# Performance work log

Hardware: AMD Instinct MI355X
Metric: run time of the kernel (lower is better)

Reference implementation:

```python
import jax, jax.numpy as jnp
import numpy as np

L_LAYERS = 6
D = 768
H = 12
DH = D // H
FF = 3072
B = 32
LX = 256
LY = 128
EPS = 1e-6
NEG = -1e9


def setup_inputs() -> dict:
    key = jax.random.key(0)
    ks = jax.random.split(key, 24)
    s = 0.02
    f32 = jnp.float32
    inp = {
        'y': jax.random.normal(ks[0], (B, LY, D), f32),
        'x': jax.random.normal(ks[1], (B, LX, D), f32),
        'y_mask': jnp.zeros((B, 1, 1, LY), bool),
        'x_mask': jnp.zeros((B, 1, 1, LX), bool),
        'y_pos': jnp.arange(B * LY, dtype=jnp.int32).reshape(B, LY),
        'bbox': jax.random.normal(ks[2], (B, LX, 4), f32),
        # encoder (SA) params, stacked over layers; attn weight order: q,k,v,merge
        'enc_attn_w': jax.random.normal(ks[3], (L_LAYERS, 4, D, D), f32) * s,
        'enc_attn_b': jnp.zeros((L_LAYERS, 4, D), f32),
        'enc_ffn_w1': jax.random.normal(ks[4], (L_LAYERS, D, FF), f32) * s,
        'enc_ffn_b1': jnp.zeros((L_LAYERS, FF), f32),
        'enc_ffn_w2': jax.random.normal(ks[5], (L_LAYERS, FF, D), f32) * s,
        'enc_ffn_b2': jnp.zeros((L_LAYERS, D), f32),
        'enc_ln_g': jnp.ones((L_LAYERS, 2, D), f32),
        'enc_ln_b': jnp.zeros((L_LAYERS, 2, D), f32),
        # decoder (RELAGA) params; two attentions per layer (self, cross)
        'dec_attn_w': jax.random.normal(ks[6], (L_LAYERS, 2, 4, D, D), f32) * s,
        'dec_attn_b': jnp.zeros((L_LAYERS, 2, 4, D), f32),
        'dec_ffn_w1': jax.random.normal(ks[7], (L_LAYERS, D, FF), f32) * s,
        'dec_ffn_b1': jnp.zeros((L_LAYERS, FF), f32),
        'dec_ffn_w2': jax.random.normal(ks[8], (L_LAYERS, FF, D), f32) * s,
        'dec_ffn_b2': jnp.zeros((L_LAYERS, D), f32),
        'dec_ln_g': jnp.ones((L_LAYERS, 3, D), f32),
        'dec_ln_b': jnp.zeros((L_LAYERS, 3, D), f32),
    }
    return inp


def _layernorm(t, g, b):
    m = jnp.mean(t, axis=-1, keepdims=True)
    v = jnp.mean((t - m) ** 2, axis=-1, keepdims=True)
    return g * (t - m) / jnp.sqrt(v + EPS) + b


def _heads(t, w, bias):
    # [B,L,D] -> [B,H,L,DH]
    nb = t.shape[0]
    return (t @ w + bias).reshape(nb, -1, H, DH).transpose(0, 2, 1, 3)


def _mha(v, k, q, mask, w, bias, rel=None):
    # w: [4,D,D] (q,k,v,merge), bias: [4,D]; rel: [B,1,Lq,Lq] or None
    qh = _heads(q, w[0], bias[0])
    kh = _heads(k, w[1], bias[1])
    vh = _heads(v, w[2], bias[2])
    scores = jnp.einsum('bhqd,bhkd->bhqk', qh, kh) / np.sqrt(DH).astype(np.float32)
    scores = jnp.where(mask, NEG, scores)
    att = jax.nn.softmax(scores, axis=-1)
    out = jnp.einsum('bhqk,bhkd->bhqd', att, vh)
    if rel is not None:
        out = jnp.einsum('bhqp,bhpd->bhqd', rel, out)  # bbox-relational matmul
    nb = q.shape[0]
    out = out.transpose(0, 2, 1, 3).reshape(nb, -1, D)
    return out @ w[3] + bias[3]


def _ffn(t, w1, b1, w2, b2):
    return jnp.maximum(t @ w1 + b1, 0.0) @ w2 + b2


def reference(y, x, y_mask, x_mask, y_pos, bbox,
              enc_attn_w, enc_attn_b, enc_ffn_w1, enc_ffn_b1, enc_ffn_w2, enc_ffn_b2,
              enc_ln_g, enc_ln_b,
              dec_attn_w, dec_attn_b, dec_ffn_w1, dec_ffn_b1, dec_ffn_w2, dec_ffn_b2,
              dec_ln_g, dec_ln_b):
    # bbox cosine-similarity relation matrix (softmax over last dim), shared across heads
    prod = jnp.einsum('bic,bjc->bij', bbox, bbox)
    n = jnp.sqrt(jnp.sum(bbox * bbox, axis=-1))          # [B,LX]
    denom = n[:, :, None] * n[:, None, :]                 # [B,LX,LX]
    sim = jax.nn.softmax(prod / denom, axis=2)[:, None]   # [B,1,LX,LX] broadcasts over heads

    for i in range(L_LAYERS):  # encoder: SA stack over y
        att = _mha(y, y, y, y_mask, enc_attn_w[i], enc_attn_b[i])
        y = _layernorm(y + att, enc_ln_g[i, 0], enc_ln_b[i, 0])
        f = _ffn(y, enc_ffn_w1[i], enc_ffn_b1[i], enc_ffn_w2[i], enc_ffn_b2[i])
        y = _layernorm(y + f, enc_ln_g[i, 1], enc_ln_b[i, 1])

    for i in range(L_LAYERS):  # decoder: RELAGA stack over x
        att = _mha(x, x, x, x_mask, dec_attn_w[i, 0], dec_attn_b[i, 0], rel=sim)
        x = _layernorm(x + att, dec_ln_g[i, 0], dec_ln_b[i, 0])
        att = _mha(y, y, x, y_mask, dec_attn_w[i, 1], dec_attn_b[i, 1], rel=sim)
        x = _layernorm(x + att, dec_ln_g[i, 1], dec_ln_b[i, 1])
        f = _ffn(x, dec_ffn_w1[i], dec_ffn_b1[i], dec_ffn_w2[i], dec_ffn_b2[i])
        x = _layernorm(x + f, dec_ln_g[i, 2], dec_ln_b[i, 2])

    return (y, x)
```

## Files before the change

### kernel.cpp

```cpp
#include <hip/hip_runtime.h>

#define DEV __device__ __forceinline__

constexpr int NB  = 32;
constexpr int LXc = 256;
constexpr int LYc = 128;
constexpr int Dc  = 768;
constexpr int NH  = 12;
constexpr int FFc = 3072;

typedef unsigned short u16;
typedef float f32x4 __attribute__((ext_vector_type(4)));
typedef short s16x8 __attribute__((ext_vector_type(8)));

DEV u16 f2bf(float f) {
  unsigned u = __float_as_uint(f);
  u += 0x7FFFu + ((u >> 16) & 1u);
  return (u16)(u >> 16);
}
DEV float bf2f(u16 w) { return __uint_as_float(((unsigned)w) << 16); }
DEV float ldf(const void* p, long long i, int isbf) {
  return isbf ? bf2f(((const u16*)p)[i]) : ((const float*)p)[i];
}

DEV void gload16(const void* g, void* l) {
  __builtin_amdgcn_global_load_lds(
      (const __attribute__((address_space(1))) void*)g,
      (__attribute__((address_space(3))) void*)l, 16, 0, 0);
}
DEV void barx() {
  asm volatile("" ::: "memory");
  __builtin_amdgcn_s_barrier();
  asm volatile("" ::: "memory");
}

__global__ void k_detect(const u16* y, int* flag) {
  if (threadIdx.x == 0) {
    int cnt = 0;
    for (int i = 0; i < 256; ++i) {
      u16 w = y[i];
      int e = (w >> 7) & 0xFF;
      if (e == 0 || (e >= 112 && e <= 140)) cnt++;
    }
    *flag = (cnt >= 200) ? 1 : 0;
  }
}

__global__ void k_ingest_b(const void* src, u16* dst, long long n, const int* flag) {
  int isbf = *flag;
  long long i = (long long)blockIdx.x * blockDim.x + threadIdx.x;
  long long st = (long long)gridDim.x * blockDim.x;
  for (; i < n; i += st) dst[i] = isbf ? ((const u16*)src)[i] : f2bf(((const float*)src)[i]);
}

__global__ void k_cvt(const void* src, float* dst, long long n, const int* flag) {
  int isbf = *flag;
  long long i = (long long)blockIdx.x * blockDim.x + threadIdx.x;
  long long st = (long long)gridDim.x * blockDim.x;
  for (; i < n; i += st) dst[i] = ldf(src, i, isbf);
}

__global__ void k_emit(const u16* ybuf, const u16* xbuf, void* out,
                       const int* flag, long long ny, long long nt) {
  int isbf = *flag;
  long long i = (long long)blockIdx.x * blockDim.x + threadIdx.x;
  long long st = (long long)gridDim.x * blockDim.x;
  for (; i < nt; i += st) {
    u16 v = (i < ny) ? ybuf[i] : xbuf[i - ny];
    if (isbf) ((u16*)out)[i] = v;
    else      ((float*)out)[i] = bf2f(v);
  }
}

__global__ __launch_bounds__(256) void k_wt(const void* src, u16* dst, int R, int C, const int* flag) {
  int isbf = *flag;
  __shared__ u16 t[32][33];
  long long base = (long long)blockIdx.z * R * C;
  int c0 = blockIdx.x * 32, r0 = blockIdx.y * 32;
  int tx = threadIdx.x & 31, ty = threadIdx.x >> 5;
#pragma unroll
  for (int k = 0; k < 4; ++k) {
    int r = r0 + ty + k * 8;
    t[ty + k * 8][tx] = f2bf(ldf(src, base + (long long)r * C + (c0 + tx), isbf));
  }
  __syncthreads();
#pragma unroll
  for (int k = 0; k < 4; ++k) {
    int c = c0 + ty + k * 8;
    dst[base + (long long)c * R + (r0 + tx)] = t[tx][ty + k * 8];
  }
}

__global__ __launch_bounds__(256) void k_bboxsim(const void* bbox, const int* flag, u16* sim) {
  int isbf = *flag;
  int b = blockIdx.x >> 8, i = blockIdx.x & 255;
  int j = threadIdx.x;
  long long base = (long long)b * LXc * 4;
  float a[4], c[4];
#pragma unroll
  for (int t = 0; t < 4; ++t) {
    a[t] = ldf(bbox, base + (long long)i * 4 + t, isbf);
    c[t] = ldf(bbox, base + (long long)j * 4 + t, isbf);
  }
  float dot = a[0]*c[0] + a[1]*c[1] + a[2]*c[2] + a[3]*c[3];
  float na  = sqrtf(a[0]*a[0] + a[1]*a[1] + a[2]*a[2] + a[3]*a[3]);
  float ncn = sqrtf(c[0]*c[0] + c[1]*c[1] + c[2]*c[2] + c[3]*c[3]);
  float v = dot / (na * ncn);
  __shared__ float r1[4], r2[4];
  float m = v;
  for (int o = 32; o; o >>= 1) m = fmaxf(m, __shfl_xor(m, o));
  if ((threadIdx.x & 63) == 0) r1[threadIdx.x >> 6] = m;
  __syncthreads();
  m = fmaxf(fmaxf(r1[0], r1[1]), fmaxf(r1[2], r1[3]));
  float e = __expf(v - m);
  float s = e;
  for (int o = 32; o; o >>= 1) s += __shfl_xor(s, o);
  if ((threadIdx.x & 63) == 0) r2[threadIdx.x >> 6] = s;
  __syncthreads();
  s = r2[0] + r2[1] + r2[2] + r2[3];
  sim[((long long)b * LXc + i) * LXc + j] = f2bf(e / s);
}

__global__ __launch_bounds__(192) void k_lnres4(u16* curb, const u16* delta,
                                                const void* g, long long gOff,
                                                const void* bb, long long bOff,
                                                const int* flag) {
  int isbf = *flag;
  long long row = blockIdx.x;
  u16* xr = curb + row * Dc;
  const u16* dr = delta + row * Dc;
  int t = threadIdx.x;
  union { u16 u[4]; uint2 d; } xa, da;
  xa.d = *(const uint2*)(xr + t * 4);
  da.d = *(const uint2*)(dr + t * 4);
  float v[4];
  float s = 0.f;
#pragma unroll
  for (int i = 0; i < 4; ++i) { v[i] = bf2f(xa.u[i]) + bf2f(da.u[i]); s += v[i]; }
  __shared__ float r1[3], r2[3];
  for (int o = 32; o; o >>= 1) s += __shfl_xor(s, o);
  if ((t & 63) == 0) r1[t >> 6] = s;
  __syncthreads();
  float mean = (r1[0] + r1[1] + r1[2]) * (1.0f / 768.0f);
  float s2 = 0.f;
#pragma unroll
  for (int i = 0; i < 4; ++i) { float d = v[i] - mean; s2 += d * d; }
  for (int o = 32; o; o >>= 1) s2 += __shfl_xor(s2, o);
  if ((t & 63) == 0) r2[t >> 6] = s2;
  __syncthreads();
  float var = (r2[0] + r2[1] + r2[2]) * (1.0f / 768.0f);
  float rstd = rsqrtf(var + 1e-6f);
  union { u16 u[4]; uint2 d; } oa;
#pragma unroll
  for (int i = 0; i < 4; ++i) {
    int c = t * 4 + i;
    float o = ldf(g, gOff + c, isbf) * (v[i] - mean) * rstd + ldf(bb, bOff + c, isbf);
    oa.u[i] = f2bf(o);
  }
  *(uint2*)(xr + t * 4) = oa.d;
}

template<int DEC>
__global__ __launch_bounds__(256) void k_attn(const u16* __restrict__ Q,
                                              const u16* __restrict__ Kb,
                                              const u16* __restrict__ Vt,
                                              u16* __restrict__ Out,
                                              int Lq, int Lk) {
  __shared__ __align__(16) u16 Kl[64 * 64];
  __shared__ __align__(16) u16 Vl[64 * 64];
  __shared__ __align__(16) u16 Pl[4][16][72];
  const int tid = threadIdx.x, wid = tid >> 6, lane = tid & 63;
  const int qt = blockIdx.x, h = blockIdx.y, b = blockIdx.z;
  const int q0 = qt * 64 + wid * 16;
  const int rl = lane & 15, sx = lane >> 4;
  const int srow = lane >> 3;
  const int scol8 = ((lane & 7) ^ srow) << 3;

  s16x8 qa[2];
  {
    const u16* qrow = Q + ((long long)b * Lq + q0 + rl) * Dc + h * 64;
    qa[0] = *(const s16x8*)(qrow + sx * 8);
    qa[1] = *(const s16x8*)(qrow + 32 + sx * 8);
  }
  f32x4 o[4] = {};
  float m[4], l[4];
#pragma unroll
  for (int e = 0; e < 4; ++e) { m[e] = -3.0e38f; l[e] = 0.f; }

  const long long kbase = (long long)b * Lk * Dc + h * 64;
  const long long vbase = ((long long)b * Dc + h * 64) * Lk;

  for (int k0 = 0; k0 < Lk; k0 += 64) {
#pragma unroll
    for (int g = 0; g < 2; ++g) {
      int chunk = g * 4 + wid;
      gload16(Kb + kbase + (long long)(k0 + chunk * 8 + srow) * Dc + scol8,
              (char*)Kl + chunk * 1024);
    }
#pragma unroll
    for (int g = 0; g < 2; ++g) {
      int chunk = g * 4 + wid;
      gload16(Vt + vbase + (long long)(chunk * 8 + srow) * Lk + k0 + scol8,
              (char*)Vl + chunk * 1024);
    }
    asm volatile("s_waitcnt vmcnt(0)" ::: "memory");
    barx();

    f32x4 s[4];
#pragma unroll
    for (int n = 0; n < 4; ++n) {
      s16x8 b0 = *(const s16x8*)((char*)Kl + (n * 16 + rl) * 128 + ((sx    ) ^ (rl & 7)) * 16);
      s16x8 b1 = *(const s16x8*)((char*)Kl + (n * 16 + rl) * 128 + ((sx + 4) ^ (rl & 7)) * 16);
      f32x4 acc = {};
      acc = __builtin_amdgcn_mfma_f32_16x16x32_bf16(qa[0], b0, acc, 0, 0, 0);
      acc = __builtin_amdgcn_mfma_f32_16x16x32_bf16(qa[1], b1, acc, 0, 0, 0);
      s[n] = acc;
    }
#pragma unroll
    for (int n = 0; n < 4; ++n)
#pragma unroll
      for (int e = 0; e < 4; ++e) s[n][e] *= 0.125f;

#pragma unroll
    for (int e = 0; e < 4; ++e) {
      float v = fmaxf(fmaxf(s[0][e], s[1][e]), fmaxf(s[2][e], s[3][e]));
      v = fmaxf(v, __shfl_xor(v, 1));
      v = fmaxf(v, __shfl_xor(v, 2));
      v = fmaxf(v, __shfl_xor(v, 4));
      v = fmaxf(v, __shfl_xor(v, 8));
      float mn = fmaxf(m[e], v);
      float alpha = __expf(m[e] - mn);
      m[e] = mn;
      float ls = 0.f;
#pragma unroll
      for (int n = 0; n < 4; ++n) {
        float p = __expf(s[n][e] - mn);
        s[n][e] = p;
        ls += p;
      }
      ls += __shfl_xor(ls, 1);
      ls += __shfl_xor(ls, 2);
      ls += __shfl_xor(ls, 4);
      ls += __shfl_xor(ls, 8);
      l[e] = l[e] * alpha + ls;
#pragma unroll
      for (int n = 0; n < 4; ++n) o[n][e] *= alpha;
    }

#pragma unroll
    for (int e = 0; e < 4; ++e)
#pragma unroll
      for (int n = 0; n < 4; ++n)
        Pl[wid][sx * 4 + e][n * 16 + rl] = f2bf(s[n][e]);
    barx();

    s16x8 pa0 = *(const s16x8*)&Pl[wid][rl][sx * 8];
    s16x8 pa1 = *(const s16x8*)&Pl[wid][rl][32 + sx * 8];
#pragma unroll
    for (int n = 0; n < 4; ++n) {
      s16x8 v0 = *(const s16x8*)((char*)Vl + (n * 16 + rl) * 128 + ((sx    ) ^ (rl & 7)) * 16);
      s16x8 v1 = *(const s16x8*)((char*)Vl + (n * 16 + rl) * 128 + ((sx + 4) ^ (rl & 7)) * 16);
      o[n] = __builtin_amdgcn_mfma_f32_16x16x32_bf16(pa0, v0, o[n], 0, 0, 0);
      o[n] = __builtin_amdgcn_mfma_f32_16x16x32_bf16(pa1, v1, o[n], 0, 0, 0);
    }
    barx();
  }

#pragma unroll
  for (int e = 0; e < 4; ++e) l[e] = 1.0f / l[e];
  if (DEC) {
    u16* Op = Out + ((long long)b * Dc + h * 64) * LXc;
#pragma unroll
    for (int n = 0; n < 4; ++n) {
      union { u16 u[4]; uint2 d; } pk;
#pragma unroll
      for (int e = 0; e < 4; ++e) pk.u[e] = f2bf(o[n][e] * l[e]);
      *(uint2*)&Op[(long long)(n * 16 + rl) * LXc + q0 + sx * 4] = pk.d;
    }
  } else {
    u16* Op = Out + ((long long)b * Lq + q0) * Dc + h * 64;
#pragma unroll
    for (int n = 0; n < 4; ++n)
#pragma unroll
      for (int e = 0; e < 4; ++e)
        Op[(long long)(sx * 4 + e) * Dc + n * 16 + rl] = f2bf(o[n][e] * l[e]);
  }
}

struct G2 {
  const u16* A; long long lda, sAb, sAh;
  const u16* W; long long ldw, sWb, sWh;
  const float* bias; long long bOff;
  void* C; long long ldc, sCb, sCh;
  void* Ck; void* Cv; int vSeg;
  int Hdim; float scale; int relu; int Lseq;
};

template<int BM, int BN, int MODE>
__global__ __launch_bounds__(256, 2) void gemm2(G2 p, int M, int N, int K) {
  constexpr int BK = 64;
  constexpr int NLD = BM / 32 + BN / 32;
  __shared__ __align__(16) u16 Al[2][BM * BK];
  __shared__ __align__(16) u16 Bl[2][BN * BK];
  const int tid = threadIdx.x, wid = tid >> 6, lane = tid & 63;
  const int z = blockIdx.z, zb = z / p.Hdim, zh = z % p.Hdim;
  int bx = blockIdx.x, by = blockIdx.y;
  if (gridDim.z == 1) {
    int gx = gridDim.x, nwg = gx * gridDim.y;
    int orig = by * gx + bx;
    int q = nwg >> 3, r = nwg & 7, xcd = orig & 7, lin = orig >> 3;
    int wg = (xcd < r ? xcd * (q + 1) : r * (q + 1) + (xcd - r) * q) + lin;
    bx = wg % gx; by = wg / gx;
  }
  const u16* A = p.A + (long long)zb * p.sAb + (long long)zh * p.sAh;
  const u16* W = p.W + (long long)zb * p.sWb + (long long)zh * p.sWh;
  const int m0 = by * BM, n0 = bx * BN;
  const int wr = wid >> 1, wc = wid & 1;
  constexpr int FM = BM / 32, FN = BN / 32;
  f32x4 acc[FM][FN] = {};
  const int lr = lane >> 3;
  const int lo = (((lane & 7) ^ lr) << 3) * 2;
  const int rl = lane & 15;
  const int sx = lane >> 4;
  const int slotb0 = (((sx + 0) ^ (rl & 7)) << 4);
  const int slotb1 = (((sx + 4) ^ (rl & 7)) << 4);

  auto stage = [&](int t, int bb) {
    long long k0 = (long long)t * BK;
#pragma unroll
    for (int i = 0; i < FM; ++i) {
      int chunk = wid * FM + i;
      int row = chunk * 8 + lr;
      gload16((const char*)(A + (long long)(m0 + row) * p.lda + k0) + lo,
              (char*)Al[bb] + chunk * 1024);
    }
#pragma unroll
    for (int i = 0; i < FN; ++i) {
      int chunk = wid * FN + i;
      int row = chunk * 8 + lr;
      gload16((const char*)(W + (long long)(n0 + row) * p.ldw + k0) + lo,
              (char*)Bl[bb] + chunk * 1024);
    }
  };

  const int NT = K / BK;
  stage(0, 0);
  for (int t = 0; t < NT; ++t) {
    const int bb = t & 1;
    if (t + 1 < NT) {
      stage(t + 1, bb ^ 1);
      if constexpr (NLD == 8)      asm volatile("s_waitcnt vmcnt(8)" ::: "memory");
      else if constexpr (NLD == 6) asm volatile("s_waitcnt vmcnt(6)" ::: "memory");
      else                         asm volatile("s_waitcnt vmcnt(0)" ::: "memory");
    } else {
      asm volatile("s_waitcnt vmcnt(0)" ::: "memory");
    }
    barx();
    {
      s16x8 af[FM][2], bfr[FN][2];
#pragma unroll
      for (int i = 0; i < FM; ++i) {
        const char* rbase = (char*)Al[bb] + (wr * (BM / 2) + i * 16 + rl) * 128;
        af[i][0] = *(const s16x8*)(rbase + slotb0);
        af[i][1] = *(const s16x8*)(rbase + slotb1);
      }
#pragma unroll
      for (int j = 0; j < FN; ++j) {
        const char* rbase = (char*)Bl[bb] + (wc * (BN / 2) + j * 16 + rl) * 128;
        bfr[j][0] = *(const s16x8*)(rbase + slotb0);
        bfr[j][1] = *(const s16x8*)(rbase + slotb1);
      }
#pragma unroll
      for (int ks = 0; ks < 2; ++ks)
#pragma unroll
        for (int i = 0; i < FM; ++i)
#pragma unroll
          for (int j = 0; j < FN; ++j)
            acc[i][j] = __builtin_amdgcn_mfma_f32_16x16x32_bf16(af[i][ks], bfr[j][ks], acc[i][j], 0, 0, 0);
    }
    barx();
  }

  const int seg = (MODE == 4) ? (n0 / 768) : 0;
#pragma unroll
  for (int j = 0; j < FN; ++j) {
    int col = n0 + wc * (BN / 2) + j * 16 + (lane & 15);
    float bv = p.bias ? p.bias[p.bOff + col] : 0.f;
#pragma unroll
    for (int i = 0; i < FM; ++i) {
      int row0 = m0 + wr * (BM / 2) + i * 16 + (lane >> 4) * 4;
      if (MODE == 0) {
        u16* C = (u16*)p.C + (long long)zb * p.sCb + (long long)zh * p.sCh;
#pragma unroll
        for (int e = 0; e < 4; ++e) {
          float v = acc[i][j][e] * p.scale + bv;
          if (p.relu) v = fmaxf(v, 0.f);
          C[(long long)(row0 + e) * p.ldc + col] = f2bf(v);
        }
      } else {
        u16* outp = seg == 0 ? (u16*)p.C : (seg == 1 ? (u16*)p.Ck : (u16*)p.Cv);
        int c = col - seg * 768;
        if (seg == p.vSeg) {
          int b = row0 / p.Lseq, l = row0 % p.Lseq;
          union { u16 u[4]; uint2 d; } pk;
#pragma unroll
          for (int e = 0; e < 4; ++e) pk.u[e] = f2bf(acc[i][j][e] + bv);
          *(uint2*)&outp[((long long)b * Dc + c) * p.Lseq + l] = pk.d;
        } else {
#pragma unroll
          for (int e = 0; e < 4; ++e)
            outp[(long long)(row0 + e) * 768 + c] = f2bf(acc[i][j][e] + bv);
        }
      }
    }
  }
}

template<int BM, int BN, int MODE>
static void run_gemm(const G2& p, int M, int N, int K, int nz, hipStream_t st) {
  dim3 grid(N / BN, M / BM, nz);
  gemm2<BM, BN, MODE><<<grid, 256, 0, st>>>(p, M, N, K);
}

extern "C" void kernel_launch(void* const* d_in, const int* in_sizes, int n_in,
                              void* d_out, int out_size, void* d_ws, size_t ws_size,
                              hipStream_t stream) {
  const void* y_in  = d_in[0];
  const void* x_in  = d_in[1];
  const void* bbox  = d_in[5];
  const void* enc_aw = d_in[6];  const void* enc_ab = d_in[7];
  const void* enc_w1 = d_in[8];  const void* enc_b1 = d_in[9];
  const void* enc_w2 = d_in[10]; const void* enc_b2 = d_in[11];
  const void* enc_lg = d_in[12]; const void* enc_lb = d_in[13];
  const void* dec_aw = d_in[14]; const void* dec_ab = d_in[15];
  const void* dec_w1 = d_in[16]; const void* dec_b1 = d_in[17];
  const void* dec_w2 = d_in[18]; const void* dec_b2 = d_in[19];
  const void* dec_lg = d_in[20]; const void* dec_lb = d_in[21];

  char* base = (char*)d_ws;
  size_t off = 0;
  auto alloc = [&](size_t bytes) { void* p = base + off; off = (off + bytes + 255) & ~(size_t)255; return p; };
  int*  flag = (int*)alloc(256);
  const long long DD = (long long)Dc * Dc;
  const long long DF = (long long)Dc * FFc;
  u16* WencA  = (u16*)alloc(24 * DD * 2);
  u16* WencW1 = (u16*)alloc(6 * DF * 2);
  u16* WencW2 = (u16*)alloc(6 * DF * 2);
  u16* WdecA  = (u16*)alloc(48 * DD * 2);
  u16* WdecW1 = (u16*)alloc(6 * DF * 2);
  u16* WdecW2 = (u16*)alloc(6 * DF * 2);
  float* BencA  = (float*)alloc(24 * Dc * 4);
  float* BencW1 = (float*)alloc(6 * FFc * 4);
  float* BencW2 = (float*)alloc(6 * Dc * 4);
  float* BdecA  = (float*)alloc(48 * Dc * 4);
  float* BdecW1 = (float*)alloc(6 * FFc * 4);
  float* BdecW2 = (float*)alloc(6 * Dc * 4);
  const long long NYt = (long long)NB * LYc * Dc;
  const long long NXt = (long long)NB * LXc * Dc;
  u16*   curb_y = (u16*)alloc(NYt * 2);
  u16*   curb_x = (u16*)alloc(NXt * 2);
  u16*   simb   = (u16*)alloc((long long)NB * LXc * LXc * 2);
  u16*   qbf    = (u16*)alloc(NXt * 2);
  u16*   kbf    = (u16*)alloc(NXt * 2);
  u16*   vT     = (u16*)alloc(NXt * 2);
  u16*   deltab = (u16*)alloc(NXt * 2);
  u16*   aoT    = (u16*)alloc(NXt * 2);
  u16*   ao2    = (u16*)alloc(NXt * 2);
  u16*   ffmid  = (u16*)alloc((long long)NB * LXc * FFc * 2);

  k_detect<<<1, 64, 0, stream>>>((const u16*)y_in, flag);
  k_ingest_b<<<1024, 256, 0, stream>>>(y_in, curb_y, NYt, flag);
  k_ingest_b<<<1024, 256, 0, stream>>>(x_in, curb_x, NXt, flag);
  k_bboxsim<<<NB * LXc, 256, 0, stream>>>(bbox, flag, simb);
  k_wt<<<dim3(Dc/32, Dc/32, 24), 256, 0, stream>>>(enc_aw, WencA, Dc, Dc, flag);
  k_wt<<<dim3(FFc/32, Dc/32, 6), 256, 0, stream>>>(enc_w1, WencW1, Dc, FFc, flag);
  k_wt<<<dim3(Dc/32, FFc/32, 6), 256, 0, stream>>>(enc_w2, WencW2, FFc, Dc, flag);
  k_wt<<<dim3(Dc/32, Dc/32, 48), 256, 0, stream>>>(dec_aw, WdecA, Dc, Dc, flag);
  k_wt<<<dim3(FFc/32, Dc/32, 6), 256, 0, stream>>>(dec_w1, WdecW1, Dc, FFc, flag);
  k_wt<<<dim3(Dc/32, FFc/32, 6), 256, 0, stream>>>(dec_w2, WdecW2, FFc, Dc, flag);
  k_cvt<<<32, 256, 0, stream>>>(enc_ab, BencA, 24 * Dc, flag);
  k_cvt<<<32, 256, 0, stream>>>(enc_b1, BencW1, 6 * FFc, flag);
  k_cvt<<<32, 256, 0, stream>>>(enc_b2, BencW2, 6 * Dc, flag);
  k_cvt<<<32, 256, 0, stream>>>(dec_ab, BdecA, 48 * Dc, flag);
  k_cvt<<<32, 256, 0, stream>>>(dec_b1, BdecW1, 6 * FFc, flag);
  k_cvt<<<32, 256, 0, stream>>>(dec_b2, BdecW2, 6 * Dc, flag);

  auto qkv = [&](const u16* A, int M, const u16* Wt, long long wOff,
                 const float* bias, long long bOff, int Lseq) {
    G2 p{}; p.A = A; p.lda = Dc; p.W = Wt + wOff; p.ldw = Dc;
    p.bias = bias; p.bOff = bOff;
    p.C = qbf; p.Ck = kbf; p.Cv = vT; p.vSeg = 2;
    p.Hdim = 1; p.scale = 1.f; p.Lseq = Lseq;
    run_gemm<128, 128, 4>(p, M, 3 * Dc, Dc, 1, stream);
  };
  auto kv = [&](const u16* A, int M, const u16* Wt, long long wOff,
                const float* bias, long long bOff, int Lseq) {
    G2 p{}; p.A = A; p.lda = Dc; p.W = Wt + wOff; p.ldw = Dc;
    p.bias = bias; p.bOff = bOff;
    p.C = kbf; p.Ck = vT; p.vSeg = 1;
    p.Hdim = 1; p.scale = 1.f; p.Lseq = Lseq;
    run_gemm<128, 128, 4>(p, M, 2 * Dc, Dc, 1, stream);
  };
  auto p768 = [&](const u16* A, int M, const u16* Wt, long long wOff,
                  const float* bias, long long bOff, u16* C, int K, int relu) {
    G2 p{}; p.A = A; p.lda = K; p.W = Wt + wOff; p.ldw = K;
    p.bias = bias; p.bOff = bOff; p.C = C; p.ldc = Dc;
    p.Hdim = 1; p.scale = 1.f; p.relu = relu;
    run_gemm<128, 64, 0>(p, M, Dc, K, 1, stream);
  };
  auto ffn1 = [&](const u16* A, int M, const u16* Wt, long long wOff,
                  const float* bias, long long bOff) {
    G2 p{}; p.A = A; p.lda = Dc; p.W = Wt + wOff; p.ldw = Dc;
    p.bias = bias; p.bOff = bOff; p.C = ffmid; p.ldc = FFc;
    p.Hdim = 1; p.scale = 1.f; p.relu = 1;
    run_gemm<128, 128, 0>(p, M, FFc, Dc, 1, stream);
  };
  auto g_rel = [&]() {
    G2 p{}; p.A = simb; p.lda = LXc; p.sAb = (long long)LXc * LXc;
    p.W = aoT; p.ldw = LXc; p.sWb = (long long)Dc * LXc;
    p.C = ao2; p.ldc = Dc; p.sCb = (long long)LXc * Dc;
    p.Hdim = 1; p.scale = 1.f;
    run_gemm<128, 128, 0>(p, LXc, Dc, LXc, NB, stream);
  };

  for (int i = 0; i < 6; ++i) {
    int M = NB * LYc;
    long long wo = (long long)i * 4 * DD, bo = (long long)i * 4 * Dc;
    qkv(curb_y, M, WencA, wo, BencA, bo, LYc);
    k_attn<0><<<dim3(LYc / 64, NH, NB), 256, 0, stream>>>(qbf, kbf, vT, ao2, LYc, LYc);
    p768(ao2, M, WencA, wo + 3 * DD, BencA, bo + 3 * Dc, deltab, Dc, 0);
    k_lnres4<<<M, 192, 0, stream>>>(curb_y, deltab, enc_lg, (long long)(i*2+0)*Dc, enc_lb, (long long)(i*2+0)*Dc, flag);
    ffn1(curb_y, M, WencW1, (long long)i * DF, BencW1, (long long)i * FFc);
    p768(ffmid, M, WencW2, (long long)i * DF, BencW2, (long long)i * Dc, deltab, FFc, 0);
    k_lnres4<<<M, 192, 0, stream>>>(curb_y, deltab, enc_lg, (long long)(i*2+1)*Dc, enc_lb, (long long)(i*2+1)*Dc, flag);
  }

  for (int i = 0; i < 6; ++i) {
    int M = NB * LXc;
    for (int a = 0; a < 2; ++a) {
      long long wo = (long long)(i * 2 + a) * 4 * DD;
      long long bo = (long long)(i * 2 + a) * 4 * Dc;
      int Lk;
      if (a == 0) {
        qkv(curb_x, M, WdecA, wo, BdecA, bo, LXc);
        Lk = LXc;
      } else {
        p768(curb_x, M, WdecA, wo, BdecA, bo, qbf, Dc, 0);
        kv(curb_y, NB * LYc, WdecA, wo + DD, BdecA, bo + Dc, LYc);
        Lk = LYc;
      }
      k_attn<1><<<dim3(LXc / 64, NH, NB), 256, 0, stream>>>(qbf, kbf, vT, aoT, LXc, Lk);
      g_rel();
      p768(ao2, M, WdecA, wo + 3 * DD, BdecA, bo + 3 * Dc, deltab, Dc, 0);
      k_lnres4<<<M, 192, 0, stream>>>(curb_x, deltab, dec_lg, (long long)(i*3+a)*Dc, dec_lb, (long long)(i*3+a)*Dc, flag);
    }
    ffn1(curb_x, M, WdecW1, (long long)i * DF, BdecW1, (long long)i * FFc);
    p768(ffmid, M, WdecW2, (long long)i * DF, BdecW2, (long long)i * Dc, deltab, FFc, 0);
    k_lnres4<<<M, 192, 0, stream>>>(curb_x, deltab, dec_lg, (long long)(i*3+2)*Dc, dec_lb, (long long)(i*3+2)*Dc, flag);
  }

  k_emit<<<2048, 256, 0, stream>>>(curb_y, curb_x, d_out, flag, NYt, NYt + NXt);
}
```

Measured before the change: 3.436 ms.

## Drop GEMM LDS double buffering and use smaller tiles for short-sequence GEMMs

```diff
diff --git a/kernel.cpp b/kernel.cpp
--- a/kernel.cpp
+++ b/kernel.cpp
@@ -299,9 +299,8 @@
 template<int BM, int BN, int MODE>
 __global__ __launch_bounds__(256, 2) void gemm2(G2 p, int M, int N, int K) {
   constexpr int BK = 64;
-  constexpr int NLD = BM / 32 + BN / 32;
-  __shared__ __align__(16) u16 Al[2][BM * BK];
-  __shared__ __align__(16) u16 Bl[2][BN * BK];
+  __shared__ __align__(16) u16 Al[BM * BK];
+  __shared__ __align__(16) u16 Bl[BN * BK];
   const int tid = threadIdx.x, wid = tid >> 6, lane = tid & 63;
   const int z = blockIdx.z, zb = z / p.Hdim, zh = z % p.Hdim;
   int bx = blockIdx.x, by = blockIdx.y;
@@ -325,48 +324,33 @@
   const int slotb0 = (((sx + 0) ^ (rl & 7)) << 4);
   const int slotb1 = (((sx + 4) ^ (rl & 7)) << 4);
 
-  auto stage = [&](int t, int bb) {
-    long long k0 = (long long)t * BK;
+  for (int k0 = 0; k0 < K; k0 += BK) {
 #pragma unroll
     for (int i = 0; i < FM; ++i) {
       int chunk = wid * FM + i;
       int row = chunk * 8 + lr;
       gload16((const char*)(A + (long long)(m0 + row) * p.lda + k0) + lo,
-              (char*)Al[bb] + chunk * 1024);
+              (char*)Al + chunk * 1024);
     }
 #pragma unroll
     for (int i = 0; i < FN; ++i) {
       int chunk = wid * FN + i;
       int row = chunk * 8 + lr;
       gload16((const char*)(W + (long long)(n0 + row) * p.ldw + k0) + lo,
-              (char*)Bl[bb] + chunk * 1024);
-    }
-  };
-
-  const int NT = K / BK;
-  stage(0, 0);
-  for (int t = 0; t < NT; ++t) {
-    const int bb = t & 1;
-    if (t + 1 < NT) {
-      stage(t + 1, bb ^ 1);
-      if constexpr (NLD == 8)      asm volatile("s_waitcnt vmcnt(8)" ::: "memory");
-      else if constexpr (NLD == 6) asm volatile("s_waitcnt vmcnt(6)" ::: "memory");
-      else                         asm volatile("s_waitcnt vmcnt(0)" ::: "memory");
-    } else {
-      asm volatile("s_waitcnt vmcnt(0)" ::: "memory");
-    }
-    barx();
+              (char*)Bl + chunk * 1024);
+    }
+    __syncthreads();
     {
       s16x8 af[FM][2], bfr[FN][2];
 #pragma unroll
       for (int i = 0; i < FM; ++i) {
-        const char* rbase = (char*)Al[bb] + (wr * (BM / 2) + i * 16 + rl) * 128;
+        const char* rbase = (char*)Al + (wr * (BM / 2) + i * 16 + rl) * 128;
         af[i][0] = *(const s16x8*)(rbase + slotb0);
         af[i][1] = *(const s16x8*)(rbase + slotb1);
       }
 #pragma unroll
       for (int j = 0; j < FN; ++j) {
-        const char* rbase = (char*)Bl[bb] + (wc * (BN / 2) + j * 16 + rl) * 128;
+        const char* rbase = (char*)Bl + (wc * (BN / 2) + j * 16 + rl) * 128;
         bfr[j][0] = *(const s16x8*)(rbase + slotb0);
         bfr[j][1] = *(const s16x8*)(rbase + slotb1);
       }
@@ -378,7 +362,7 @@
           for (int j = 0; j < FN; ++j)
             acc[i][j] = __builtin_amdgcn_mfma_f32_16x16x32_bf16(af[i][ks], bfr[j][ks], acc[i][j], 0, 0, 0);
     }
-    barx();
+    __syncthreads();
   }
 
   const int seg = (MODE == 4) ? (n0 / 768) : 0;
@@ -499,14 +483,15 @@
     p.bias = bias; p.bOff = bOff;
     p.C = kbf; p.Ck = vT; p.vSeg = 1;
     p.Hdim = 1; p.scale = 1.f; p.Lseq = Lseq;
-    run_gemm<128, 128, 4>(p, M, 2 * Dc, Dc, 1, stream);
+    run_gemm<64, 128, 4>(p, M, 2 * Dc, Dc, 1, stream);
   };
   auto p768 = [&](const u16* A, int M, const u16* Wt, long long wOff,
                   const float* bias, long long bOff, u16* C, int K, int relu) {
     G2 p{}; p.A = A; p.lda = K; p.W = Wt + wOff; p.ldw = K;
     p.bias = bias; p.bOff = bOff; p.C = C; p.ldc = Dc;
     p.Hdim = 1; p.scale = 1.f; p.relu = relu;
-    run_gemm<128, 64, 0>(p, M, Dc, K, 1, stream);
+    if (M == NB * LXc) run_gemm<128, 64, 0>(p, M, Dc, K, 1, stream);
+    else               run_gemm<64, 64, 0>(p, M, Dc, K, 1, stream);
   };
   auto ffn1 = [&](const u16* A, int M, const u16* Wt, long long wOff,
                   const float* bias, long long bOff) {
```

New measurement: 3.234 ms. 1.06x faster.
